# Kernel optimization log

Hardware: AMD Instinct MI355X
Metric: run time of the kernel (lower is better)

The kernel has to match this reference:

```python
import jax, jax.numpy as jnp
import numpy as np


def setup_inputs() -> dict:
    key = jax.random.key(0)
    k1, k2, k3, k4 = jax.random.split(key, 4)
    B, I, O, N, T = 4096, 512, 64, 32, 4
    E = N * T
    x = jax.random.normal(k1, (B, I), dtype=jnp.float32)
    dst_state = jax.random.uniform(k2, (B, N), dtype=jnp.float32)
    type_state = jax.random.uniform(k3, (B, T), dtype=jnp.float32)
    # orthogonal init with gain=0.01 approximated by small random weights; bias=0
    W = jax.random.normal(k4, (E, I, O), dtype=jnp.float32) * 0.01
    b = jnp.zeros((E, O), dtype=jnp.float32)
    return {"x": x, "dst_state": dst_state, "type_state": type_state, "W": W, "b": b}


def reference(x, dst_state, type_state, W, b):
    # gating weights: outer product of dst_state [B,N] and type_state [B,T],
    # flattened to [B, E] with E = N*T (row-major, matching torch view)
    B = x.shape[0]
    g = (dst_state[:, :, None] * type_state[:, None, :]).reshape(B, -1)  # [B,E]
    # per-expert linear then gated sum over experts, fused via einsum
    logits = jnp.einsum("bi,eio,be->bo", x, W, g) + jnp.einsum("be,eo->bo", g, b)
    # torch.distributions.Categorical(logits=...) normalizes logits
    return jax.nn.log_softmax(logits, axis=-1)
```

## Files before the change

kernel.cpp:

```cpp
#include <hip/hip_runtime.h>
#include <hip/hip_bf16.h>

typedef __bf16 bf16x8 __attribute__((ext_vector_type(8)));
typedef float  f32x4  __attribute__((ext_vector_type(4)));

#define B_SZ 4096
#define I_SZ 512
#define O_SZ 64
#define E_SZ 128
#define BM   256
#define G_EXP 8
#define EG_N  16
#define MT_N  16

__global__ void prep_xg(const float* __restrict__ x, __bf16* __restrict__ xb,
                        const float* __restrict__ ds, const float* __restrict__ ts,
                        float* __restrict__ gT) {
  int i = blockIdx.x * 256 + threadIdx.x;
  float4 v = ((const float4*)x)[i];
  union { __bf16 h[4]; ushort4 u4; } pk;
  pk.h[0] = (__bf16)v.x; pk.h[1] = (__bf16)v.y;
  pk.h[2] = (__bf16)v.z; pk.h[3] = (__bf16)v.w;
  ((ushort4*)xb)[i] = pk.u4;
  int e = i >> 12, b = i & 4095;
  gT[i] = ds[b * 32 + (e >> 2)] * ts[b * 4 + (e & 3)];
}

__global__ void prep_w(const float* __restrict__ W, __bf16* __restrict__ wt) {
  __shared__ __bf16 tile[64][66];
  int e  = blockIdx.x >> 3;
  int it = blockIdx.x & 7;
  const float* src = W + (size_t)e * I_SZ * O_SZ + (size_t)it * 64 * O_SZ;
  #pragma unroll
  for (int s = 0; s < 16; ++s) {
    int idx = s * 256 + threadIdx.x;
    int r = idx >> 6, o = idx & 63;
    tile[o][r] = (__bf16)src[idx];
  }
  __syncthreads();
  __bf16* dst = wt + (size_t)e * O_SZ * I_SZ + it * 64;
  #pragma unroll
  for (int s = 0; s < 4; ++s) {
    int idx = s * 256 + threadIdx.x;
    int o = idx >> 4, c = (idx & 15) << 2;
    union { __bf16 h[4]; ushort4 u4; } q;
    q.h[0] = tile[o][c + 0]; q.h[1] = tile[o][c + 1];
    q.h[2] = tile[o][c + 2]; q.h[3] = tile[o][c + 3];
    *(ushort4*)&dst[(size_t)o * I_SZ + c] = q.u4;
  }
}

__global__ __launch_bounds__(512, 2)
void mtc_gemm(const __bf16* __restrict__ xb, const __bf16* __restrict__ wt,
              const float* __restrict__ gT, const float* __restrict__ bias,
              float* __restrict__ partials) {
  __shared__ __align__(16) __bf16 wsh[2][O_SZ * I_SZ];
  __shared__ float gsh[G_EXP][BM];

  const int tid  = threadIdx.x;
  const int wave = tid >> 6;
  const int lane = tid & 63;

  int bid = (int)blockIdx.x;
  bid = (bid & 7) * 32 + (bid >> 3);
  const int mtile = bid & 15;
  const int eg    = bid >> 4;
  const int row0  = mtile * BM;
  const int e0    = eg * G_EXP;

  auto stage2 = [&](int sbuf, int e, int s) {
    const __bf16* wsrc = wt + (size_t)(e0 + e) * O_SZ * I_SZ;
    #pragma unroll
    for (int ii = 0; ii < 2; ++ii) {
      int o = (s * 2 + ii) * 8 + wave;
      int q = lane ^ (o & 7);
      __builtin_amdgcn_global_load_lds(
          (const __attribute__((address_space(1))) void*)(wsrc + (size_t)o * I_SZ + q * 8),
          (__attribute__((address_space(3))) void*)(&wsh[sbuf][o * I_SZ]),
          16, 0, 0);
    }
  };

  #pragma unroll
  for (int s = 0; s < 4; ++s) stage2(0, 0, s);

  for (int idx = tid; idx < G_EXP * BM; idx += 512)
    gsh[idx >> 8][idx & 255] =
        gT[(size_t)(e0 + (idx >> 8)) * B_SZ + row0 + (idx & 255)];

  bf16x8 af[2][16];
  {
    const __bf16* xr = xb + (size_t)(row0 + wave * 32 + (lane & 15)) * I_SZ
                          + (lane >> 4) * 8;
    #pragma unroll
    for (int mf = 0; mf < 2; ++mf)
      #pragma unroll
      for (int j = 0; j < 16; ++j)
        af[mf][j] = *(const bf16x8*)(xr + mf * 16 * I_SZ + j * 32);
  }

  __syncthreads();

  f32x4 logits[2][4] = {};
  int buf = 0;
  for (int e = 0; e < G_EXP; ++e) {
    float bv[4];
    #pragma unroll
    for (int nf = 0; nf < 4; ++nf)
      bv[nf] = bias[(size_t)(e0 + e) * O_SZ + nf * 16 + (lane & 15)];
    f32x4 acc[2][4];
    #pragma unroll
    for (int mf = 0; mf < 2; ++mf)
      #pragma unroll
      for (int nf = 0; nf < 4; ++nf)
        acc[mf][nf] = (f32x4){bv[nf], bv[nf], bv[nf], bv[nf]};

    const __bf16* wb = &wsh[buf][0];
    #pragma unroll
    for (int s = 0; s < 4; ++s) {
      if (e < G_EXP - 1) stage2(buf ^ 1, e + 1, s);
      __builtin_amdgcn_s_setprio(1);
      #pragma unroll
      for (int jj = 0; jj < 4; ++jj) {
        const int j = s * 4 + jj;
        bf16x8 bfr[4];
        #pragma unroll
        for (int nf = 0; nf < 4; ++nf) {
          int o  = nf * 16 + (lane & 15);
          int q  = j * 4 + (lane >> 4);
          int ph = q ^ (o & 7);
          bfr[nf] = *(const bf16x8*)(wb + (size_t)o * I_SZ + ph * 8);
        }
        #pragma unroll
        for (int nf = 0; nf < 4; ++nf)
          #pragma unroll
          for (int mf = 0; mf < 2; ++mf)
            acc[mf][nf] = __builtin_amdgcn_mfma_f32_16x16x32_bf16(
                af[mf][j], bfr[nf], acc[mf][nf], 0, 0, 0);
      }
      __builtin_amdgcn_s_setprio(0);
      __builtin_amdgcn_s_barrier();
    }

    f32x4 gq[2];
    #pragma unroll
    for (int mf = 0; mf < 2; ++mf)
      gq[mf] = *(const f32x4*)&gsh[e][wave * 32 + mf * 16 + (lane >> 4) * 4];
    #pragma unroll
    for (int mf = 0; mf < 2; ++mf)
      #pragma unroll
      for (int nf = 0; nf < 4; ++nf)
        #pragma unroll
        for (int rg = 0; rg < 4; ++rg)
          logits[mf][nf][rg] += gq[mf][rg] * acc[mf][nf][rg];

    asm volatile("s_waitcnt vmcnt(0)" ::: "memory");
    __builtin_amdgcn_s_barrier();
    buf ^= 1;
  }

  float* pout = partials + (size_t)eg * B_SZ * O_SZ + (size_t)row0 * O_SZ;
  #pragma unroll
  for (int mf = 0; mf < 2; ++mf)
    #pragma unroll
    for (int nf = 0; nf < 4; ++nf)
      #pragma unroll
      for (int rg = 0; rg < 4; ++rg) {
        int r = wave * 32 + mf * 16 + ((lane >> 4) << 2) + rg;
        int o = nf * 16 + (lane & 15);
        pout[(size_t)r * O_SZ + o] = logits[mf][nf][rg];
      }
}

__global__ __launch_bounds__(256)
void mtc_reduce(const float* __restrict__ partials, float* __restrict__ out) {
  int wave = threadIdx.x >> 6, lane = threadIdx.x & 63;
  int r = blockIdx.x * 4 + wave;
  float s = 0.f;
  #pragma unroll
  for (int k = 0; k < EG_N; ++k)
    s += partials[(size_t)k * B_SZ * O_SZ + (size_t)r * O_SZ + lane];
  float m = s;
  #pragma unroll
  for (int off = 32; off; off >>= 1) m = fmaxf(m, __shfl_xor(m, off));
  float ex = expf(s - m), sum = ex;
  #pragma unroll
  for (int off = 32; off; off >>= 1) sum += __shfl_xor(sum, off);
  out[(size_t)r * O_SZ + lane] = s - m - logf(sum);
}

extern "C" void kernel_launch(void* const* d_in, const int* in_sizes, int n_in,
                              void* d_out, int out_size, void* d_ws, size_t ws_size,
                              hipStream_t stream) {
  const float* x    = (const float*)d_in[0];
  const float* ds   = (const float*)d_in[1];
  const float* ts   = (const float*)d_in[2];
  const float* W    = (const float*)d_in[3];
  const float* bias = (const float*)d_in[4];
  float* out = (float*)d_out;

  char* w = (char*)d_ws;
  __bf16* xb      = (__bf16*)(w);
  __bf16* wt      = (__bf16*)(w + (4ull  << 20));
  float*  gT      = (float*) (w + (12ull << 20));
  float*  parts   = (float*) (w + (14ull << 20));

  prep_xg   <<<2048, 256, 0, stream>>>(x, xb, ds, ts, gT);
  prep_w    <<<1024, 256, 0, stream>>>(W, wt);
  mtc_gemm  <<< 256, 512, 0, stream>>>(xb, wt, gT, bias, parts);
  mtc_reduce<<<1024, 256, 0, stream>>>(parts, out);
}
```

Before: 63.53 us.

## Restructure weight LDS layout into k-chunks and prefetch next expert ahead

Splits the per-expert weight tile in shared memory into eight 64-wide k-chunks, each row swizzled within a 64-element chunk, and issues all of the next expert's loads at the top of the iteration. The wait is a partial vmcnt so compute on the current buffer overlaps the in-flight prefetch, with one barrier per expert instead of four. Bias loads for all eight experts are hoisted before the loop. This cuts barrier count and sync stalls but raises register use for the hoisted bias values, and it relies on the vmcnt count matching the eight issued loads per stage.

```diff
diff --git a/kernel.cpp b/kernel.cpp
--- a/kernel.cpp
+++ b/kernel.cpp
@@ -54,7 +54,7 @@
 void mtc_gemm(const __bf16* __restrict__ xb, const __bf16* __restrict__ wt,
               const float* __restrict__ gT, const float* __restrict__ bias,
               float* __restrict__ partials) {
-  __shared__ __align__(16) __bf16 wsh[2][O_SZ * I_SZ];
+  __shared__ __align__(16) __bf16 wsh[2][8][64 * 64];
   __shared__ float gsh[G_EXP][BM];
 
   const int tid  = threadIdx.x;
@@ -68,21 +68,20 @@
   const int row0  = mtile * BM;
   const int e0    = eg * G_EXP;
 
-  auto stage2 = [&](int sbuf, int e, int s) {
+  auto stage = [&](int sbuf, int e) {
     const __bf16* wsrc = wt + (size_t)(e0 + e) * O_SZ * I_SZ;
-    #pragma unroll
-    for (int ii = 0; ii < 2; ++ii) {
-      int o = (s * 2 + ii) * 8 + wave;
-      int q = lane ^ (o & 7);
+    int o = tid >> 3, p = tid & 7;
+    int sl = p ^ (o & 7);
+    #pragma unroll
+    for (int kc = 0; kc < 8; ++kc) {
       __builtin_amdgcn_global_load_lds(
-          (const __attribute__((address_space(1))) void*)(wsrc + (size_t)o * I_SZ + q * 8),
-          (__attribute__((address_space(3))) void*)(&wsh[sbuf][o * I_SZ]),
+          (const __attribute__((address_space(1))) void*)(wsrc + (size_t)o * I_SZ + kc * 64 + sl * 8),
+          (__attribute__((address_space(3))) void*)(&wsh[sbuf][kc][wave * 512]),
           16, 0, 0);
     }
   };
 
-  #pragma unroll
-  for (int s = 0; s < 4; ++s) stage2(0, 0, s);
+  stage(0, 0);
 
   for (int idx = tid; idx < G_EXP * BM; idx += 512)
     gsh[idx >> 8][idx & 255] =
@@ -99,48 +98,53 @@
         af[mf][j] = *(const bf16x8*)(xr + mf * 16 * I_SZ + j * 32);
   }
 
+  float bv[G_EXP][4];
+  #pragma unroll
+  for (int e = 0; e < G_EXP; ++e)
+    #pragma unroll
+    for (int nf = 0; nf < 4; ++nf)
+      bv[e][nf] = bias[(size_t)(e0 + e) * O_SZ + nf * 16 + (lane & 15)];
+
   __syncthreads();
 
   f32x4 logits[2][4] = {};
   int buf = 0;
   for (int e = 0; e < G_EXP; ++e) {
-    float bv[4];
-    #pragma unroll
-    for (int nf = 0; nf < 4; ++nf)
-      bv[nf] = bias[(size_t)(e0 + e) * O_SZ + nf * 16 + (lane & 15)];
+    if (e < G_EXP - 1) {
+      stage(buf ^ 1, e + 1);
+      asm volatile("s_waitcnt vmcnt(8)" ::: "memory");
+    } else {
+      asm volatile("s_waitcnt vmcnt(0)" ::: "memory");
+    }
+    __builtin_amdgcn_s_barrier();
+
     f32x4 acc[2][4];
     #pragma unroll
     for (int mf = 0; mf < 2; ++mf)
       #pragma unroll
       for (int nf = 0; nf < 4; ++nf)
-        acc[mf][nf] = (f32x4){bv[nf], bv[nf], bv[nf], bv[nf]};
-
-    const __bf16* wb = &wsh[buf][0];
-    #pragma unroll
-    for (int s = 0; s < 4; ++s) {
-      if (e < G_EXP - 1) stage2(buf ^ 1, e + 1, s);
-      __builtin_amdgcn_s_setprio(1);
-      #pragma unroll
-      for (int jj = 0; jj < 4; ++jj) {
-        const int j = s * 4 + jj;
-        bf16x8 bfr[4];
+        acc[mf][nf] = (f32x4){bv[e][nf], bv[e][nf], bv[e][nf], bv[e][nf]};
+
+    __builtin_amdgcn_s_setprio(1);
+    #pragma unroll
+    for (int j = 0; j < 16; ++j) {
+      const __bf16* wb = &wsh[buf][j >> 1][0];
+      bf16x8 bfr[4];
+      #pragma unroll
+      for (int nf = 0; nf < 4; ++nf) {
+        int o  = nf * 16 + (lane & 15);
+        int q  = (j & 1) * 4 + (lane >> 4);
+        int ph = q ^ (o & 7);
+        bfr[nf] = *(const bf16x8*)(wb + o * 64 + ph * 8);
+      }
+      #pragma unroll
+      for (int nf = 0; nf < 4; ++nf)
         #pragma unroll
-        for (int nf = 0; nf < 4; ++nf) {
-          int o  = nf * 16 + (lane & 15);
-          int q  = j * 4 + (lane >> 4);
-          int ph = q ^ (o & 7);
-          bfr[nf] = *(const bf16x8*)(wb + (size_t)o * I_SZ + ph * 8);
-        }
-        #pragma unroll
-        for (int nf = 0; nf < 4; ++nf)
-          #pragma unroll
-          for (int mf = 0; mf < 2; ++mf)
-            acc[mf][nf] = __builtin_amdgcn_mfma_f32_16x16x32_bf16(
-                af[mf][j], bfr[nf], acc[mf][nf], 0, 0, 0);
-      }
-      __builtin_amdgcn_s_setprio(0);
-      __builtin_amdgcn_s_barrier();
+        for (int mf = 0; mf < 2; ++mf)
+          acc[mf][nf] = __builtin_amdgcn_mfma_f32_16x16x32_bf16(
+              af[mf][j], bfr[nf], acc[mf][nf], 0, 0, 0);
     }
+    __builtin_amdgcn_s_setprio(0);
 
     f32x4 gq[2];
     #pragma unroll
@@ -154,7 +158,6 @@
         for (int rg = 0; rg < 4; ++rg)
           logits[mf][nf][rg] += gq[mf][rg] * acc[mf][nf][rg];
 
-    asm volatile("s_waitcnt vmcnt(0)" ::: "memory");
     __builtin_amdgcn_s_barrier();
     buf ^= 1;
   }
```

Measured after the change: 83.86 us. +32.0%, slower.
